# Kernel optimization log

Measured on AMD Instinct MI355X. Metric: run time of the kernel, lower is better.

The kernel has to match this reference:

```python
import jax, jax.numpy as jnp
import numpy as np

TOP_K = 2

def setup_inputs() -> dict:
    key = jax.random.key(0)
    k1, k2, k3, k4 = jax.random.split(key, 4)
    B, S, D, F, E = 4, 2048, 1024, 4096, 8
    x = jax.random.normal(k1, (B, S, D), dtype=jnp.float32)
    gate_w = jax.random.normal(k2, (D, E), dtype=jnp.float32) * 0.02
    w1 = jax.random.normal(k3, (E, D, F), dtype=jnp.float32) * 0.02
    w2 = jax.random.normal(k4, (E, F, D), dtype=jnp.float32) * 0.02
    return {"x": x, "gate_w": gate_w, "w1": w1, "w2": w2}

def reference(x, gate_w, w1, w2):
    # Eval-mode MoE: no router noise, dropout is identity, aux_loss=None.
    B, S, D = x.shape
    E = gate_w.shape[1]
    T = B * S
    xt = x.reshape(T, D)                                  # [T, D]
    logits = xt @ gate_w                                   # [T, E]
    topk_logits, topk_idx = jax.lax.top_k(logits, TOP_K)   # [T, k]
    topk_w = jax.nn.softmax(topk_logits, axis=-1)          # [T, k]
    # Dense combine weights: top_k indices are distinct, so scatter-set is exact.
    combine = jnp.zeros((T, E), dtype=x.dtype).at[
        jnp.arange(T)[:, None], topk_idx
    ].set(topk_w)                                          # [T, E]
    out = jnp.zeros_like(xt)
    for e in range(E):  # fixed small expert count
        h = jax.nn.silu(xt @ w1[e]) @ w2[e]                # [T, D]
        out = out + combine[:, e:e + 1] * h
    return out.reshape(B, S, D)
```

## Files before the change

kernel.cpp:

```cpp
#include <hip/hip_runtime.h>
#include <cstdio>

typedef unsigned short u16;
typedef unsigned int u32;
typedef __attribute__((ext_vector_type(8))) short bf16x8;
typedef __attribute__((ext_vector_type(4))) float f32x4;

static constexpr int T = 8192;
static constexpr int D = 1024;
static constexpr int F = 4096;
static constexpr int E = 8;

__device__ __forceinline__ u16 f2b(float f) {
  u32 u = __float_as_uint(f);
  u32 r = (u + 0x7fffu + ((u >> 16) & 1u)) >> 16;
  return (u16)r;
}
__device__ __forceinline__ float b2f(u16 u) {
  return __uint_as_float(((u32)u) << 16);
}

__device__ __forceinline__ void gload16(const void* g, void* l) {
  typedef const __attribute__((address_space(1))) void* gp_t;
  typedef __attribute__((address_space(3))) void* lp_t;
  __builtin_amdgcn_global_load_lds((gp_t)(uintptr_t)g, (lp_t)(uintptr_t)l, 16, 0, 0);
}

template<int R, int C>
__global__ void transpose_cvt_kernel(const float* __restrict__ in, u16* __restrict__ outp) {
  __shared__ float tile[64][65];
  const size_t base = (size_t)blockIdx.z * R * C;
  const int r0 = blockIdx.y * 64, c0 = blockIdx.x * 64;
  const int tx = threadIdx.x & 63, tg = threadIdx.x >> 6;
#pragma unroll
  for (int i = 0; i < 16; ++i) {
    int r = i * 4 + tg;
    tile[r][tx] = in[base + (size_t)(r0 + r) * C + (c0 + tx)];
  }
  __syncthreads();
  const int l32 = threadIdx.x & 31, g8 = threadIdx.x >> 5;
#pragma unroll
  for (int i = 0; i < 8; ++i) {
    int rp = i * 8 + g8;
    u16 v0 = f2b(tile[l32 * 2][rp]);
    u16 v1 = f2b(tile[l32 * 2 + 1][rp]);
    *(u32*)(outp + base + (size_t)(c0 + rp) * R + (r0 + l32 * 2)) = (u32)v0 | ((u32)v1 << 16);
  }
}

__global__ void gate_kernel(const float* __restrict__ x, const float* __restrict__ gw,
                            u16* __restrict__ xb,
                            int* __restrict__ tki, float* __restrict__ tkw) {
  const int lane = threadIdx.x & 63;
  const int t = blockIdx.x * 4 + (threadIdx.x >> 6);
  const float* xr = x + (size_t)t * D + lane * 16;

  float xv[16];
#pragma unroll
  for (int i = 0; i < 4; ++i) {
    float4 v = ((const float4*)xr)[i];
    xv[i * 4 + 0] = v.x; xv[i * 4 + 1] = v.y; xv[i * 4 + 2] = v.z; xv[i * 4 + 3] = v.w;
  }
  union { u16 s[16]; uint4 q[2]; } pk;
#pragma unroll
  for (int j = 0; j < 16; ++j) pk.s[j] = f2b(xv[j]);
  uint4* xbo = (uint4*)(xb + (size_t)t * D + lane * 16);
  xbo[0] = pk.q[0]; xbo[1] = pk.q[1];

  double acc[8] = {0, 0, 0, 0, 0, 0, 0, 0};
  const float4* gwp = (const float4*)(gw + (size_t)(lane * 16) * 8);
#pragma unroll
  for (int j = 0; j < 16; ++j) {
    double xd = (double)xv[j];
    float4 g0 = gwp[j * 2], g1 = gwp[j * 2 + 1];
    acc[0] += xd * (double)g0.x; acc[1] += xd * (double)g0.y;
    acc[2] += xd * (double)g0.z; acc[3] += xd * (double)g0.w;
    acc[4] += xd * (double)g1.x; acc[5] += xd * (double)g1.y;
    acc[6] += xd * (double)g1.z; acc[7] += xd * (double)g1.w;
  }
#pragma unroll
  for (int s = 1; s < 64; s <<= 1) {
#pragma unroll
    for (int e = 0; e < 8; ++e) acc[e] += __shfl_xor(acc[e], s, 64);
  }
  if (lane == 0) {
    int i0 = 0; double l0 = acc[0];
#pragma unroll
    for (int e = 1; e < 8; ++e) if (acc[e] > l0) { l0 = acc[e]; i0 = e; }
    int i1 = -1; double l1 = -1e300;
#pragma unroll
    for (int e = 0; e < 8; ++e) if (e != i0 && acc[e] > l1) { l1 = acc[e]; i1 = e; }
    float w0 = (float)(1.0 / (1.0 + exp(l1 - l0)));
    float w1f = 1.0f - w0;
    tki[t * 2] = i0; tki[t * 2 + 1] = i1;
    tkw[t * 2] = w0; tkw[t * 2 + 1] = w1f;
  }
}

__global__ __launch_bounds__(1024) void scan_build_kernel(
    const int* __restrict__ tki, const float* __restrict__ tkw,
    int* __restrict__ offs, int* __restrict__ lst, float* __restrict__ lsw) {
  const int tid = threadIdx.x;
  const int lane = tid & 63, wv = tid >> 6;
  const int base = tid * 16;
  int e_loc[16]; float w_loc[16];
  int cnt[8] = {0, 0, 0, 0, 0, 0, 0, 0};
#pragma unroll
  for (int i = 0; i < 16; ++i) {
    e_loc[i] = tki[base + i];
    w_loc[i] = tkw[base + i];
    cnt[e_loc[i]]++;
  }
  __shared__ int wsum[8][16];
  int excl[8];
#pragma unroll
  for (int e = 0; e < 8; ++e) {
    int inc = cnt[e];
#pragma unroll
    for (int s = 1; s < 64; s <<= 1) {
      int u = __shfl_up(inc, s, 64);
      if (lane >= s) inc += u;
    }
    if (lane == 63) wsum[e][wv] = inc;
    excl[e] = inc - cnt[e];
  }
  __syncthreads();
  int wbase[8], tot[8];
#pragma unroll
  for (int e = 0; e < 8; ++e) {
    int sb = 0, st = 0;
    for (int w = 0; w < 16; ++w) { int v = wsum[e][w]; if (w < wv) sb += v; st += v; }
    wbase[e] = sb; tot[e] = st;
  }
  int eoffs[9]; eoffs[0] = 0;
#pragma unroll
  for (int e = 0; e < 8; ++e) eoffs[e + 1] = eoffs[e] + tot[e];
  if (tid == 0) {
#pragma unroll
    for (int e = 0; e <= 8; ++e) offs[e] = eoffs[e];
  }
  int pos[8];
#pragma unroll
  for (int e = 0; e < 8; ++e) pos[e] = eoffs[e] + wbase[e] + excl[e];
#pragma unroll
  for (int i = 0; i < 16; ++i) {
    int e = e_loc[i];
    int p = pos[e]++;
    lst[p] = (base + i) >> 1;
    lsw[p] = w_loc[i];
  }
}

template<int KD, int ND, bool G1>
__global__ __launch_bounds__(256, 2) void moe_gemm(
    const u16* __restrict__ Abase, const u16* __restrict__ Bt, u16* __restrict__ hOut,
    float* __restrict__ fOut,
    const int* __restrict__ offs, const int* __restrict__ lst,
    const float* __restrict__ lsw) {
  __shared__ u16 As[128 * 64];
  __shared__ u16 Bs[128 * 64];
  const int e = blockIdx.z;
  const int off = offs[e];
  const int cnt = offs[e + 1] - off;
  const int m0 = blockIdx.y * 128;
  if (m0 >= cnt) return;
  const int n0 = blockIdx.x * 128;
  const int tid = threadIdx.x;
  const int lane = tid & 63;
  const int wave = tid >> 6;
  const int wm = wave >> 1;
  const int wn = wave & 1;

  u32 asrc[4], bsrc[4];
#pragma unroll
  for (int i = 0; i < 4; ++i) {
    const int linear = i * 256 + tid;
    const int row = linear >> 3;
    const int cb = (linear & 7) * 16;
    const int scb = cb ^ ((row & 7) << 4);
    int grow = m0 + row; if (grow >= cnt) grow = cnt - 1;
    u32 arow = G1 ? (u32)lst[off + grow] : (u32)(off + grow);
    asrc[i] = arow * (u32)(KD * 2) + (u32)scb;
    u32 brow = (u32)e * (u32)ND + (u32)(n0 + row);
    bsrc[i] = brow * (u32)(KD * 2) + (u32)scb;
  }
  const char* Ac = (const char*)Abase;
  const char* Bc = (const char*)Bt;

  f32x4 acc[4][4];
#pragma unroll
  for (int i = 0; i < 4; ++i)
#pragma unroll
    for (int j = 0; j < 4; ++j) acc[i][j] = (f32x4){0.f, 0.f, 0.f, 0.f};

  const int arow_r = wm * 64 + (lane & 15);
  const int brow_r = wn * 64 + (lane & 15);
  const int koff = (lane >> 4) * 16;

  for (int kt = 0; kt < KD / 64; ++kt) {
    const u32 kb = (u32)kt * 128;
    __syncthreads();
#pragma unroll
    for (int i = 0; i < 4; ++i) {
      gload16(Ac + asrc[i] + kb, (char*)As + i * 4096 + tid * 16);
      gload16(Bc + bsrc[i] + kb, (char*)Bs + i * 4096 + tid * 16);
    }
    __syncthreads();
#pragma unroll
    for (int ks = 0; ks < 2; ++ks) {
      const int kbyte = ks * 64 + koff;
      bf16x8 af[4], bfv[4];
#pragma unroll
      for (int mf = 0; mf < 4; ++mf) {
        const int row = arow_r + mf * 16;
        af[mf] = *(const bf16x8*)((const char*)As + row * 128 + (kbyte ^ ((row & 7) << 4)));
      }
#pragma unroll
      for (int nf = 0; nf < 4; ++nf) {
        const int row = brow_r + nf * 16;
        bfv[nf] = *(const bf16x8*)((const char*)Bs + row * 128 + (kbyte ^ ((row & 7) << 4)));
      }
#pragma unroll
      for (int mf = 0; mf < 4; ++mf)
#pragma unroll
        for (int nf = 0; nf < 4; ++nf)
          acc[mf][nf] = __builtin_amdgcn_mfma_f32_16x16x32_bf16(af[mf], bfv[nf], acc[mf][nf], 0, 0, 0);
    }
  }

#pragma unroll
  for (int mf = 0; mf < 4; ++mf) {
#pragma unroll
    for (int r = 0; r < 4; ++r) {
      const int grow = m0 + wm * 64 + mf * 16 + (lane >> 4) * 4 + r;
      if (grow >= cnt) continue;
      if (G1) {
        u16* op = hOut + (size_t)(off + grow) * ND + n0 + wn * 64;
#pragma unroll
        for (int nf = 0; nf < 4; ++nf) {
          float v = acc[mf][nf][r];
          v = v / (1.f + __expf(-v));
          op[nf * 16 + (lane & 15)] = f2b(v);
        }
      } else {
        const int tok = lst[off + grow];
        const float wgt = lsw[off + grow];
        float* op = fOut + (size_t)tok * ND + n0 + wn * 64;
#pragma unroll
        for (int nf = 0; nf < 4; ++nf)
          atomicAdd(op + nf * 16 + (lane & 15), acc[mf][nf][r] * wgt);
      }
    }
  }
}

extern "C" void kernel_launch(void* const* d_in, const int* in_sizes, int n_in,
                              void* d_out, int out_size, void* d_ws, size_t ws_size,
                              hipStream_t stream) {
  const float* x  = (const float*)d_in[0];
  const float* gw = (const float*)d_in[1];
  const float* w1 = (const float*)d_in[2];
  const float* w2 = (const float*)d_in[3];
  float* outp = (float*)d_out;

  char* ws = (char*)d_ws;
  size_t o = 0;
  auto alloc = [&](size_t b) { size_t r = o; o += (b + 255) & ~(size_t)255; return r; };
  size_t offs_o   = alloc((E + 1) * 4);
  size_t tki_o    = alloc((size_t)T * 2 * 4);
  size_t tkw_o    = alloc((size_t)T * 2 * 4);
  size_t lst_o    = alloc((size_t)T * 2 * 4);
  size_t lsw_o    = alloc((size_t)T * 2 * 4);
  size_t xb_o     = alloc((size_t)T * D * 2);
  size_t w1t_o    = alloc((size_t)E * D * F * 2);
  size_t w2t_o    = alloc((size_t)E * D * F * 2);
  size_t h_o      = alloc((size_t)T * 2 * F * 2);
  if (o > ws_size) {
    fprintf(stderr, "kernel_launch: ws too small (need %zu, have %zu)\n", o, ws_size);
    return;
  }

  int*   offs    = (int*)(ws + offs_o);
  int*   tki     = (int*)(ws + tki_o);
  float* tkw     = (float*)(ws + tkw_o);
  int*   lst     = (int*)(ws + lst_o);
  float* lsw     = (float*)(ws + lsw_o);
  u16*   xb      = (u16*)(ws + xb_o);
  u16*   w1t     = (u16*)(ws + w1t_o);
  u16*   w2t     = (u16*)(ws + w2t_o);
  u16*   h       = (u16*)(ws + h_o);

  hipMemsetAsync(outp, 0, (size_t)T * D * 4, stream);
  transpose_cvt_kernel<D, F><<<dim3(F / 64, D / 64, E), 256, 0, stream>>>(w1, w1t);
  transpose_cvt_kernel<F, D><<<dim3(D / 64, F / 64, E), 256, 0, stream>>>(w2, w2t);
  gate_kernel<<<T / 4, 256, 0, stream>>>(x, gw, xb, tki, tkw);
  scan_build_kernel<<<1, 1024, 0, stream>>>(tki, tkw, offs, lst, lsw);
  moe_gemm<D, F, true><<<dim3(F / 128, T / 128, E), 256, 0, stream>>>(
      xb, w1t, h, nullptr, offs, lst, lsw);
  moe_gemm<F, D, false><<<dim3(D / 128, T / 128, E), 256, 0, stream>>>(
      h, w2t, nullptr, outp, offs, lst, lsw);
}
```

Baseline: 543.7 us.

## Widen GEMM tiles to 128x256, remap blocks, replace atomics with bf16 combine pass

```diff
diff --git a/kernel.cpp b/kernel.cpp
--- a/kernel.cpp
+++ b/kernel.cpp
@@ -99,7 +99,8 @@
 
 __global__ __launch_bounds__(1024) void scan_build_kernel(
     const int* __restrict__ tki, const float* __restrict__ tkw,
-    int* __restrict__ offs, int* __restrict__ lst, float* __restrict__ lsw) {
+    int* __restrict__ offs, int* __restrict__ lst, float* __restrict__ lsw,
+    int* __restrict__ pos_of) {
   const int tid = threadIdx.x;
   const int lane = tid & 63, wv = tid >> 6;
   const int base = tid * 16;
@@ -148,41 +149,57 @@
     int p = pos[e]++;
     lst[p] = (base + i) >> 1;
     lsw[p] = w_loc[i];
+    pos_of[base + i] = p;
   }
 }
 
 template<int KD, int ND, bool G1>
-__global__ __launch_bounds__(256, 2) void moe_gemm(
-    const u16* __restrict__ Abase, const u16* __restrict__ Bt, u16* __restrict__ hOut,
-    float* __restrict__ fOut,
+__global__ __launch_bounds__(512, 4) void moe_gemm(
+    const u16* __restrict__ Abase, const u16* __restrict__ Bt, u16* __restrict__ Out,
     const int* __restrict__ offs, const int* __restrict__ lst,
     const float* __restrict__ lsw) {
   __shared__ u16 As[128 * 64];
-  __shared__ u16 Bs[128 * 64];
+  __shared__ u16 Bs[256 * 64];
+  constexpr int NXT = ND / 256;
   const int e = blockIdx.z;
   const int off = offs[e];
   const int cnt = offs[e + 1] - off;
-  const int m0 = blockIdx.y * 128;
+  const int nmAct = (cnt + 127) >> 7;
+  const int act = nmAct * NXT;
+  const int d = (int)blockIdx.y * NXT + (int)blockIdx.x;
+  const int q8 = (act + 7) >> 3;
+  if ((d >> 3) >= q8) return;
+  const int lin = (d & 7) * q8 + (d >> 3);
+  if (lin >= act) return;
+  const int m0 = (lin % nmAct) * 128;
+  const int n0 = (lin / nmAct) * 256;
   if (m0 >= cnt) return;
-  const int n0 = blockIdx.x * 128;
+
   const int tid = threadIdx.x;
   const int lane = tid & 63;
   const int wave = tid >> 6;
-  const int wm = wave >> 1;
-  const int wn = wave & 1;
-
-  u32 asrc[4], bsrc[4];
-#pragma unroll
-  for (int i = 0; i < 4; ++i) {
-    const int linear = i * 256 + tid;
-    const int row = linear >> 3;
-    const int cb = (linear & 7) * 16;
-    const int scb = cb ^ ((row & 7) << 4);
-    int grow = m0 + row; if (grow >= cnt) grow = cnt - 1;
-    u32 arow = G1 ? (u32)lst[off + grow] : (u32)(off + grow);
-    asrc[i] = arow * (u32)(KD * 2) + (u32)scb;
-    u32 brow = (u32)e * (u32)ND + (u32)(n0 + row);
-    bsrc[i] = brow * (u32)(KD * 2) + (u32)scb;
+  const int wm = wave >> 2;
+  const int wn = wave & 3;
+
+  u32 asrc[2], bsrc[4];
+  {
+    const int rr = tid >> 3;
+    const int cb = (tid & 7) * 16;
+#pragma unroll
+    for (int i = 0; i < 2; ++i) {
+      const int row = i * 64 + rr;
+      const int scb = cb ^ ((row & 7) << 4);
+      int grow = m0 + row; if (grow >= cnt) grow = cnt - 1;
+      u32 arow = G1 ? (u32)lst[off + grow] : (u32)(off + grow);
+      asrc[i] = arow * (u32)(KD * 2) + (u32)scb;
+    }
+#pragma unroll
+    for (int i = 0; i < 4; ++i) {
+      const int row = i * 64 + rr;
+      const int scb = cb ^ ((row & 7) << 4);
+      u32 brow = (u32)e * (u32)ND + (u32)(n0 + row);
+      bsrc[i] = brow * (u32)(KD * 2) + (u32)scb;
+    }
   }
   const char* Ac = (const char*)Abase;
   const char* Bc = (const char*)Bt;
@@ -201,10 +218,11 @@
     const u32 kb = (u32)kt * 128;
     __syncthreads();
 #pragma unroll
-    for (int i = 0; i < 4; ++i) {
-      gload16(Ac + asrc[i] + kb, (char*)As + i * 4096 + tid * 16);
-      gload16(Bc + bsrc[i] + kb, (char*)Bs + i * 4096 + tid * 16);
-    }
+    for (int i = 0; i < 2; ++i)
+      gload16(Ac + asrc[i] + kb, (char*)As + i * 8192 + tid * 16);
+#pragma unroll
+    for (int i = 0; i < 4; ++i)
+      gload16(Bc + bsrc[i] + kb, (char*)Bs + i * 8192 + tid * 16);
     __syncthreads();
 #pragma unroll
     for (int ks = 0; ks < 2; ++ks) {
@@ -234,24 +252,35 @@
     for (int r = 0; r < 4; ++r) {
       const int grow = m0 + wm * 64 + mf * 16 + (lane >> 4) * 4 + r;
       if (grow >= cnt) continue;
-      if (G1) {
-        u16* op = hOut + (size_t)(off + grow) * ND + n0 + wn * 64;
-#pragma unroll
-        for (int nf = 0; nf < 4; ++nf) {
-          float v = acc[mf][nf][r];
-          v = v / (1.f + __expf(-v));
-          op[nf * 16 + (lane & 15)] = f2b(v);
-        }
-      } else {
-        const int tok = lst[off + grow];
-        const float wgt = lsw[off + grow];
-        float* op = fOut + (size_t)tok * ND + n0 + wn * 64;
-#pragma unroll
-        for (int nf = 0; nf < 4; ++nf)
-          atomicAdd(op + nf * 16 + (lane & 15), acc[mf][nf][r] * wgt);
+      const float wgt = G1 ? 1.f : lsw[off + grow];
+      u16* op = Out + (size_t)(off + grow) * ND + n0 + wn * 64;
+#pragma unroll
+      for (int nf = 0; nf < 4; ++nf) {
+        float v = acc[mf][nf][r];
+        if (G1) v = v / (1.f + __expf(-v));
+        else v *= wgt;
+        op[nf * 16 + (lane & 15)] = f2b(v);
       }
     }
   }
+}
+
+__global__ void combine_kernel(const u16* __restrict__ y, const int* __restrict__ pos_of,
+                               float* __restrict__ outp) {
+  int idx = blockIdx.x * 256 + threadIdx.x;
+  int t = idx >> 7;
+  int c = (idx & 127) * 8;
+  int p0 = pos_of[t * 2], p1 = pos_of[t * 2 + 1];
+  union { uint4 v; u16 s[8]; } a, b;
+  a.v = *(const uint4*)(y + (size_t)p0 * D + c);
+  b.v = *(const uint4*)(y + (size_t)p1 * D + c);
+  float4 r0, r1;
+  r0.x = b2f(a.s[0]) + b2f(b.s[0]); r0.y = b2f(a.s[1]) + b2f(b.s[1]);
+  r0.z = b2f(a.s[2]) + b2f(b.s[2]); r0.w = b2f(a.s[3]) + b2f(b.s[3]);
+  r1.x = b2f(a.s[4]) + b2f(b.s[4]); r1.y = b2f(a.s[5]) + b2f(b.s[5]);
+  r1.z = b2f(a.s[6]) + b2f(b.s[6]); r1.w = b2f(a.s[7]) + b2f(b.s[7]);
+  *(float4*)(outp + (size_t)t * D + c) = r0;
+  *(float4*)(outp + (size_t)t * D + c + 4) = r1;
 }
 
 extern "C" void kernel_launch(void* const* d_in, const int* in_sizes, int n_in,
@@ -271,10 +300,12 @@
   size_t tkw_o    = alloc((size_t)T * 2 * 4);
   size_t lst_o    = alloc((size_t)T * 2 * 4);
   size_t lsw_o    = alloc((size_t)T * 2 * 4);
+  size_t pos_o    = alloc((size_t)T * 2 * 4);
   size_t xb_o     = alloc((size_t)T * D * 2);
   size_t w1t_o    = alloc((size_t)E * D * F * 2);
   size_t w2t_o    = alloc((size_t)E * D * F * 2);
   size_t h_o      = alloc((size_t)T * 2 * F * 2);
+  size_t y_o      = alloc((size_t)T * 2 * D * 2);
   if (o > ws_size) {
     fprintf(stderr, "kernel_launch: ws too small (need %zu, have %zu)\n", o, ws_size);
     return;
@@ -285,18 +316,20 @@
   float* tkw     = (float*)(ws + tkw_o);
   int*   lst     = (int*)(ws + lst_o);
   float* lsw     = (float*)(ws + lsw_o);
+  int*   pos_of  = (int*)(ws + pos_o);
   u16*   xb      = (u16*)(ws + xb_o);
   u16*   w1t     = (u16*)(ws + w1t_o);
   u16*   w2t     = (u16*)(ws + w2t_o);
   u16*   h       = (u16*)(ws + h_o);
-
-  hipMemsetAsync(outp, 0, (size_t)T * D * 4, stream);
+  u16*   y       = (u16*)(ws + y_o);
+
   transpose_cvt_kernel<D, F><<<dim3(F / 64, D / 64, E), 256, 0, stream>>>(w1, w1t);
   transpose_cvt_kernel<F, D><<<dim3(D / 64, F / 64, E), 256, 0, stream>>>(w2, w2t);
   gate_kernel<<<T / 4, 256, 0, stream>>>(x, gw, xb, tki, tkw);
-  scan_build_kernel<<<1, 1024, 0, stream>>>(tki, tkw, offs, lst, lsw);
-  moe_gemm<D, F, true><<<dim3(F / 128, T / 128, E), 256, 0, stream>>>(
-      xb, w1t, h, nullptr, offs, lst, lsw);
-  moe_gemm<F, D, false><<<dim3(D / 128, T / 128, E), 256, 0, stream>>>(
-      h, w2t, nullptr, outp, offs, lst, lsw);
-}
+  scan_build_kernel<<<1, 1024, 0, stream>>>(tki, tkw, offs, lst, lsw, pos_of);
+  moe_gemm<D, F, true><<<dim3(F / 256, T / 128, E), 512, 0, stream>>>(
+      xb, w1t, h, offs, lst, lsw);
+  moe_gemm<F, D, false><<<dim3(D / 256, T / 128, E), 512, 0, stream>>>(
+      h, w2t, y, offs, lst, lsw);
+  combine_kernel<<<T * D / 8 / 256, 256, 0, stream>>>(y, pos_of, outp);
+}
```

After: 572.9 us. +5.4%, slower.
